# Kernel optimization log

Measured on AMD Instinct MI355X. Metric: run time of the kernel, lower is better.

The kernel has to match this reference:

```python
import jax, jax.numpy as jnp
import numpy as np

B, CS, CT, H, W = 16, 512, 512, 64, 64

def setup_inputs() -> dict:
    key = jax.random.key(0)
    k1, k2 = jax.random.split(key)
    x = jax.random.normal(k1, (B, CS, H, W), dtype=jnp.float32)
    # 16 Linear weights, each [out_ch, in_ch] (torch Linear layout), stacked
    Wg = jax.random.normal(k2, (16, CT, CS), dtype=jnp.float32) * (2.0 / CT) ** 0.5
    return {"x": x, "Wg": Wg}

def reference(x, Wg):
    # x: [B, Cs, H, W]; Wg: [16, Ct, Cs] indexed by phase r*4+c, r=(i%4), c=(j%4)
    # Dropout is identity in eval mode (deterministic reference).
    b, cs, h, w = x.shape
    ct = Wg.shape[1]
    Wrq = Wg.reshape(4, 4, ct, cs)               # [r, q, Ct, Cs]
    xr = x.reshape(b, cs, h // 4, 4, w // 4, 4)  # [b, c, h4, r, w4, q]
    # grouped matmul: each (r,q) phase uses its own weight
    out = jnp.einsum('bchrwq,rqoc->bohrwq', xr, Wrq)
    return out.reshape(b, ct, h, w)
```

## Files before the change

kernel.cpp:

```cpp
#include <hip/hip_runtime.h>
#include <stdint.h>


typedef __attribute__((ext_vector_type(8))) short short8;
typedef __attribute__((ext_vector_type(4))) float f32x4;

#define CS 512
#define CT 512
#define HW 4096
#define BK 32
#define MT 128
#define NR 8
#define ABYTES 32768
#define BBYTES 32768
#define BUFB (ABYTES + BBYTES)

__device__ __forceinline__ uint16_t f32_to_bf16(float f) {
    uint32_t u = __builtin_bit_cast(uint32_t, f);
    u += 0x7FFFu + ((u >> 16) & 1u);
    return (uint16_t)(u >> 16);
}

__global__ __launch_bounds__(256)
void w2_cvt(const float* __restrict__ Wg, uint16_t* __restrict__ W2) {
    int idx = (blockIdx.x * 256 + threadIdx.x) * 8;
    float4 a = *(const float4*)(Wg + idx);
    float4 b = *(const float4*)(Wg + idx + 4);
    uint16_t o[8];
    o[0]=f32_to_bf16(a.x); o[1]=f32_to_bf16(a.y); o[2]=f32_to_bf16(a.z); o[3]=f32_to_bf16(a.w);
    o[4]=f32_to_bf16(b.x); o[5]=f32_to_bf16(b.y); o[6]=f32_to_bf16(b.z); o[7]=f32_to_bf16(b.w);
    *(short8*)(W2 + idx) = *(short8*)o;
}

__global__ __launch_bounds__(256)
void xt_cvt(const float* __restrict__ x, uint16_t* __restrict__ xT) {
    const int c0 = blockIdx.x * 64;
    const int h  = blockIdx.y;
    const int b  = blockIdx.z;
    const int r = h & 3, h4 = h >> 2, rg = b * 16 + h4;
    __shared__ float L[64][65];
    const int tid = threadIdx.x;
    const int wr = tid & 15;
    const int cr = tid >> 4;
    const float* src = x + (((size_t)b * CS + c0 + cr) * 64 + h) * 64 + wr * 4;
    #pragma unroll
    for (int it = 0; it < 4; ++it) {
        float4 v = *(const float4*)(src + (size_t)it * 16 * HW);
        L[cr + it * 16][wr * 4 + 0] = v.x;
        L[cr + it * 16][wr * 4 + 1] = v.y;
        L[cr + it * 16][wr * 4 + 2] = v.z;
        L[cr + it * 16][wr * 4 + 3] = v.w;
    }
    __syncthreads();
    const int orow = tid >> 2;
    const int q = orow >> 4, w16 = orow & 15;
    const int cc = (tid & 3) * 16;
    const int w = w16 * 4 + q;
    uint16_t tmp[16];
    #pragma unroll
    for (int i = 0; i < 16; ++i) tmp[i] = f32_to_bf16(L[cc + i][w]);
    uint16_t* dst = xT + ((((size_t)(r * 4 + q) * 256 + rg) * 16 + w16) * 512 + c0 + cc);
    *(short8*)(dst)     = *(short8*)(tmp);
    *(short8*)(dst + 8) = *(short8*)(tmp + 8);
}

__global__ __launch_bounds__(512, 2)
void gwl_main(const uint16_t* __restrict__ W2, const uint16_t* __restrict__ xT,
              float* __restrict__ out) {
    const int nb = blockIdx.x;
    const int mb = blockIdx.y;
    const int r  = blockIdx.z;
    const int m0 = mb * MT;

    __shared__ __align__(16) unsigned char smem[2 * BUFB];
    float* T = (float*)smem;

    const int tid  = threadIdx.x;
    const int lane = tid & 63;
    const int wave = tid >> 6;
    const int q    = wave & 3;
    const int mw   = wave >> 2;
    const int lr = lane & 15, qd = lane >> 4;

    const int lrow = lane >> 2;
    const int swz  = ((lane & 3) ^ ((lane >> 3) & 3)) * 8;

    const uint16_t* abase = W2 + ((size_t)(r * 4 + q) * CT + m0 + mw * 64) * CS;
    const uint16_t* bbase = xT + (((size_t)(r * 4 + q) * 256 + nb * 8 + mw * 4) * 16) * 512;

    auto stage = [&](int k0, int bufn) {
        uint16_t* As = (uint16_t*)(smem + bufn * BUFB) + (q * 128 + mw * 64) * 32;
        uint16_t* Bs = (uint16_t*)(smem + bufn * BUFB + ABYTES) + (q * 128 + mw * 64) * 32;
        #pragma unroll
        for (int t = 0; t < 4; ++t) {
            const uint16_t* asrc = abase + (size_t)(t * 16 + lrow) * CS + k0 + swz;
            __builtin_amdgcn_global_load_lds(
                (const __attribute__((address_space(1))) void*)asrc,
                (__attribute__((address_space(3))) void*)(As + t * 512), 16, 0, 0);
        }
        #pragma unroll
        for (int t = 0; t < 4; ++t) {
            const uint16_t* bsrc = bbase + ((size_t)t * 16 + lrow) * 512 + k0 + swz;
            __builtin_amdgcn_global_load_lds(
                (const __attribute__((address_space(1))) void*)bsrc,
                (__attribute__((address_space(3))) void*)(Bs + t * 512), 16, 0, 0);
        }
    };

    f32x4 acc[4][8] = {};

    stage(0, 0);
    stage(BK, 1);
    asm volatile("s_waitcnt vmcnt(8)" ::: "memory");
    __builtin_amdgcn_s_barrier();

    const int rdswz = (qd ^ ((lr >> 1) & 3)) * 8;
    for (int k = 0; k < 16; ++k) {
        const int buf = k & 1;
        const uint16_t* Asq = (const uint16_t*)(smem + buf * BUFB)
                              + (q * 128 + mw * 64) * 32;
        const uint16_t* Bsq = (const uint16_t*)(smem + buf * BUFB + ABYTES)
                              + q * 128 * 32;
        short8 afr[4], bfr[8];
        #pragma unroll
        for (int i = 0; i < 4; ++i)
            afr[i] = *(const short8*)(Asq + (i * 16 + lr) * 32 + rdswz);
        #pragma unroll
        for (int j = 0; j < 8; ++j)
            bfr[j] = *(const short8*)(Bsq + (j * 16 + lr) * 32 + rdswz);
        asm volatile("s_waitcnt lgkmcnt(0)" ::: "memory");
        __builtin_amdgcn_sched_barrier(0);
        __builtin_amdgcn_s_barrier();
        if (k < 14) stage((k + 2) * BK, buf);

        __builtin_amdgcn_s_setprio(1);
        #pragma unroll
        for (int i = 0; i < 4; ++i)
            #pragma unroll
            for (int j = 0; j < 8; ++j)
                acc[i][j] = __builtin_amdgcn_mfma_f32_16x16x32_bf16(
                    afr[i], bfr[j], acc[i][j], 0, 0, 0);
        __builtin_amdgcn_s_setprio(0);

        if (k < 15) {
            if (k < 14) asm volatile("s_waitcnt vmcnt(8)" ::: "memory");
            else        asm volatile("s_waitcnt vmcnt(0)" ::: "memory");
            __builtin_amdgcn_s_barrier();
        }
    }

    const int m16s = tid >> 5;
    const int rs   = (tid >> 2) & 7;
    const int ws   = (tid & 3) * 16;
    const int rgs  = nb * NR + rs;
    const int obb  = rgs >> 4;
    const int oh4  = rgs & 15;
    #pragma unroll
    for (int ic = 0; ic < 8; ++ic) {
        __syncthreads();
        if (mw == (ic >> 2)) {
            const int i = ic & 3;
            #pragma unroll
            for (int j = 0; j < 8; ++j)
                #pragma unroll
                for (int g = 0; g < 4; ++g)
                    T[((qd * 4 + g) * 8 + j) * 68 + lr * 4 + q] = acc[i][j][g];
        }
        __syncthreads();
        float* op = out + ((size_t)obb * CT + m0 + ic * 16 + m16s) * HW
                        + (oh4 * 4 + r) * 64 + ws;
        const float* tp = T + (m16s * 8 + rs) * 68 + ws;
        #pragma unroll
        for (int c = 0; c < 4; ++c)
            ((float4*)op)[c] = ((const float4*)tp)[c];
    }
}

#define BPITCH 40
#define FBUFB 73728

__global__ __launch_bounds__(512, 2)
void gwl_fb(const float* __restrict__ x, const float* __restrict__ Wg,
            float* __restrict__ out) {
    const int nb = blockIdx.x, mb = blockIdx.y, r = blockIdx.z;
    const int m0 = mb * MT;
    __shared__ __align__(16) unsigned char smem[2 * FBUFB];
    float* T = (float*)smem;
    const int tid = threadIdx.x, lane = tid & 63, wave = tid >> 6;
    const int q = wave & 3, mw = wave >> 2;
    const int lr = lane & 15, qd = lane >> 4;
    const int w16 = tid & 15, rho = (tid >> 4) & 7, kw = tid >> 7;
    const int rg = nb * NR + rho, bb = rg >> 4, h4 = rg & 15;
    const float* bbase = x + (size_t)bb * CS * HW
                           + (size_t)((h4 * 4 + r) * 64 + w16 * 4);
    float4 breg[8];
    auto loadB = [&](int k0) {
        const float* p = bbase + (size_t)(k0 + kw * 8) * HW;
        #pragma unroll
        for (int cc = 0; cc < 8; ++cc) breg[cc] = *(const float4*)(p + (size_t)cc * HW);
    };
    auto writeB = [&](uint16_t* BsD) {
        #pragma unroll
        for (int qq = 0; qq < 4; ++qq) {
            uint16_t tmp[8];
            #pragma unroll
            for (int cc = 0; cc < 8; ++cc)
                tmp[cc] = f32_to_bf16(((const float*)&breg[cc])[qq]);
            *(short8*)(BsD + (qq * 128 + rho * 16 + w16) * BPITCH + kw * 8) = *(short8*)tmp;
        }
    };
    auto stageA = [&](int k0, uint16_t* AsD) {
        const int qa = tid >> 7, rem = tid & 127;
        const int ka = rem & 7, ma = rem >> 3;
        const float* ap = Wg + ((size_t)(r * 4 + qa) * CT + m0 + ma) * CS + k0 + ka * 4;
        const int kc = (((ka >> 1) ^ ((ma >> 1) & 3)) * 8) + (ka & 1) * 4;
        #pragma unroll
        for (int it = 0; it < 8; ++it) {
            float4 v = *(const float4*)(ap + (size_t)it * 16 * CS);
            uint16_t tmp[4] = {f32_to_bf16(v.x), f32_to_bf16(v.y),
                               f32_to_bf16(v.z), f32_to_bf16(v.w)};
            *(uint64_t*)(AsD + (qa * 128 + ma + it * 16) * 32 + kc) =
                *(const uint64_t*)tmp;
        }
    };
    f32x4 acc[4][8] = {};
    {
        uint16_t* As0 = (uint16_t*)smem;
        uint16_t* Bs0 = (uint16_t*)(smem + 32768);
        loadB(0);
        stageA(0, As0);
        writeB(Bs0);
        loadB(BK);
        __syncthreads();
    }
    for (int k = 0; k < 16; ++k) {
        const uint16_t* Asq = (const uint16_t*)(smem + (k & 1) * FBUFB)
                              + (q * 128 + mw * 64) * 32;
        const uint16_t* Bsq = (const uint16_t*)(smem + (k & 1) * FBUFB + 32768)
                              + q * 128 * BPITCH;
        short8 afr[4], bfr[8];
        #pragma unroll
        for (int i = 0; i < 4; ++i)
            afr[i] = *(const short8*)(Asq + (i * 16 + lr) * 32
                                      + ((qd ^ ((lr >> 1) & 3)) * 8));
        #pragma unroll
        for (int j = 0; j < 8; ++j)
            bfr[j] = *(const short8*)(Bsq + (j * 16 + lr) * BPITCH + qd * 8);
        if (k < 15) {
            uint16_t* AsN = (uint16_t*)(smem + ((k + 1) & 1) * FBUFB);
            uint16_t* BsN = (uint16_t*)(smem + ((k + 1) & 1) * FBUFB + 32768);
            stageA((k + 1) * BK, AsN);
            writeB(BsN);
            if (k < 14) loadB((k + 2) * BK);
        }
        #pragma unroll
        for (int i = 0; i < 4; ++i)
            #pragma unroll
            for (int j = 0; j < 8; ++j)
                acc[i][j] = __builtin_amdgcn_mfma_f32_16x16x32_bf16(
                    afr[i], bfr[j], acc[i][j], 0, 0, 0);
        if (k < 15) {
            asm volatile("s_waitcnt vmcnt(0)" ::: "memory");
            asm volatile("s_waitcnt lgkmcnt(0)" ::: "memory");
            __builtin_amdgcn_s_barrier();
        }
    }
    const int m16s = tid >> 5, rs = (tid >> 2) & 7, ws = (tid & 3) * 16;
    const int rgs = nb * NR + rs, obb = rgs >> 4, oh4 = rgs & 15;
    #pragma unroll
    for (int ic = 0; ic < 8; ++ic) {
        __syncthreads();
        if (mw == (ic >> 2)) {
            const int i = ic & 3;
            #pragma unroll
            for (int j = 0; j < 8; ++j)
                #pragma unroll
                for (int g = 0; g < 4; ++g)
                    T[((qd * 4 + g) * 8 + j) * 68 + lr * 4 + q] = acc[i][j][g];
        }
        __syncthreads();
        float* op = out + ((size_t)obb * CT + m0 + ic * 16 + m16s) * HW
                        + (oh4 * 4 + r) * 64 + ws;
        const float* tp = T + (m16s * 8 + rs) * 68 + ws;
        #pragma unroll
        for (int c = 0; c < 4; ++c)
            ((float4*)op)[c] = ((const float4*)tp)[c];
    }
}

extern "C" void kernel_launch(void* const* d_in, const int* in_sizes, int n_in,
                              void* d_out, int out_size, void* d_ws, size_t ws_size,
                              hipStream_t stream) {
    const float* x  = (const float*)d_in[0];
    const float* Wg = (const float*)d_in[1];
    float* out = (float*)d_out;
    dim3 grid(32, 4, 4);
    const size_t w2_elems = (size_t)16 * 512 * 512;
    const size_t xt_elems = (size_t)4 * 4 * 256 * 16 * 512;
    if (ws_size >= (w2_elems + xt_elems) * 2) {
        uint16_t* W2 = (uint16_t*)d_ws;
        uint16_t* xT = (uint16_t*)d_ws + w2_elems;
        w2_cvt<<<2048, 256, 0, stream>>>(Wg, W2);
        xt_cvt<<<dim3(8, 64, 16), 256, 0, stream>>>(x, xT);
        gwl_main<<<grid, 512, 0, stream>>>(W2, xT, out);
    } else {
        gwl_fb<<<grid, 512, 0, stream>>>(x, Wg, out);
    }
}
```

Before: 323.2 us.

## Load MFMA operands directly from global into registers, drop LDS staging

The main GEMM kernel no longer stages A/B tiles through double-buffered LDS with global_load_lds and barriers. Each wave now loads its bf16 fragments straight from global memory into registers with a two-deep register pipeline. The block shrinks to 256 threads with a 64-row M tile, and a linearized 1024-block grid is remapped to group blocks for L2 locality. This removes LDS traffic and barrier synchronisation but relies on caches for data reuse across waves and raises register pressure.

```diff
diff --git a/kernel.cpp b/kernel.cpp
--- a/kernel.cpp
+++ b/kernel.cpp
@@ -8,12 +8,6 @@
 #define CS 512
 #define CT 512
 #define HW 4096
-#define BK 32
-#define MT 128
-#define NR 8
-#define ABYTES 32768
-#define BBYTES 32768
-#define BUFB (ABYTES + BBYTES)
 
 __device__ __forceinline__ uint16_t f32_to_bf16(float f) {
     uint32_t u = __builtin_bit_cast(uint32_t, f);
@@ -64,118 +58,94 @@
     *(short8*)(dst + 8) = *(short8*)(tmp + 8);
 }
 
-__global__ __launch_bounds__(512, 2)
+__global__ __launch_bounds__(256, 2)
 void gwl_main(const uint16_t* __restrict__ W2, const uint16_t* __restrict__ xT,
               float* __restrict__ out) {
-    const int nb = blockIdx.x;
-    const int mb = blockIdx.y;
-    const int r  = blockIdx.z;
-    const int m0 = mb * MT;
-
-    __shared__ __align__(16) unsigned char smem[2 * BUFB];
-    float* T = (float*)smem;
+    const int l  = blockIdx.x;
+    const int x3 = l & 7;
+    const int t  = l >> 3;
+    const int mb = t >> 4;
+    const int combo = (t & 15) * 8 + x3;
+    const int nb = combo >> 2;
+    const int r  = combo & 3;
+    const int m0 = mb * 64;
 
     const int tid  = threadIdx.x;
     const int lane = tid & 63;
-    const int wave = tid >> 6;
-    const int q    = wave & 3;
-    const int mw   = wave >> 2;
+    const int q    = tid >> 6;
     const int lr = lane & 15, qd = lane >> 4;
 
-    const int lrow = lane >> 2;
-    const int swz  = ((lane & 3) ^ ((lane >> 3) & 3)) * 8;
-
-    const uint16_t* abase = W2 + ((size_t)(r * 4 + q) * CT + m0 + mw * 64) * CS;
-    const uint16_t* bbase = xT + (((size_t)(r * 4 + q) * 256 + nb * 8 + mw * 4) * 16) * 512;
-
-    auto stage = [&](int k0, int bufn) {
-        uint16_t* As = (uint16_t*)(smem + bufn * BUFB) + (q * 128 + mw * 64) * 32;
-        uint16_t* Bs = (uint16_t*)(smem + bufn * BUFB + ABYTES) + (q * 128 + mw * 64) * 32;
-        #pragma unroll
-        for (int t = 0; t < 4; ++t) {
-            const uint16_t* asrc = abase + (size_t)(t * 16 + lrow) * CS + k0 + swz;
-            __builtin_amdgcn_global_load_lds(
-                (const __attribute__((address_space(1))) void*)asrc,
-                (__attribute__((address_space(3))) void*)(As + t * 512), 16, 0, 0);
-        }
-        #pragma unroll
-        for (int t = 0; t < 4; ++t) {
-            const uint16_t* bsrc = bbase + ((size_t)t * 16 + lrow) * 512 + k0 + swz;
-            __builtin_amdgcn_global_load_lds(
-                (const __attribute__((address_space(1))) void*)bsrc,
-                (__attribute__((address_space(3))) void*)(Bs + t * 512), 16, 0, 0);
-        }
-    };
+    const uint16_t* Abase = W2 + ((size_t)(r * 4 + q) * CT + m0) * CS;
+    const uint16_t* Bbase = xT + ((size_t)(r * 4 + q) * 256 + nb * 8) * 16 * 512;
+    int voA[4], voB[8];
+    #pragma unroll
+    for (int i = 0; i < 4; ++i) voA[i] = (((i * 16 + lr) * CS) + qd * 8) * 2;
+    #pragma unroll
+    for (int j = 0; j < 8; ++j) voB[j] = (((j * 16 + lr) * 512) + qd * 8) * 2;
 
     f32x4 acc[4][8] = {};
-
-    stage(0, 0);
-    stage(BK, 1);
-    asm volatile("s_waitcnt vmcnt(8)" ::: "memory");
-    __builtin_amdgcn_s_barrier();
-
-    const int rdswz = (qd ^ ((lr >> 1) & 3)) * 8;
-    for (int k = 0; k < 16; ++k) {
-        const int buf = k & 1;
-        const uint16_t* Asq = (const uint16_t*)(smem + buf * BUFB)
-                              + (q * 128 + mw * 64) * 32;
-        const uint16_t* Bsq = (const uint16_t*)(smem + buf * BUFB + ABYTES)
-                              + q * 128 * 32;
-        short8 afr[4], bfr[8];
-        #pragma unroll
-        for (int i = 0; i < 4; ++i)
-            afr[i] = *(const short8*)(Asq + (i * 16 + lr) * 32 + rdswz);
+    short8 a0[4], b0[8], a1[4], b1[8];
+
+    auto LD = [&](short8* A, short8* B, int k) {
+        const int kb = k * 64;
+        #pragma unroll
+        for (int i = 0; i < 4; ++i)
+            A[i] = *(const short8*)((const char*)Abase + voA[i] + kb);
         #pragma unroll
         for (int j = 0; j < 8; ++j)
-            bfr[j] = *(const short8*)(Bsq + (j * 16 + lr) * 32 + rdswz);
-        asm volatile("s_waitcnt lgkmcnt(0)" ::: "memory");
-        __builtin_amdgcn_sched_barrier(0);
-        __builtin_amdgcn_s_barrier();
-        if (k < 14) stage((k + 2) * BK, buf);
-
-        __builtin_amdgcn_s_setprio(1);
+            B[j] = *(const short8*)((const char*)Bbase + voB[j] + kb);
+    };
+    auto FM = [&](const short8* A, const short8* B) {
         #pragma unroll
         for (int i = 0; i < 4; ++i)
             #pragma unroll
             for (int j = 0; j < 8; ++j)
                 acc[i][j] = __builtin_amdgcn_mfma_f32_16x16x32_bf16(
-                    afr[i], bfr[j], acc[i][j], 0, 0, 0);
-        __builtin_amdgcn_s_setprio(0);
-
-        if (k < 15) {
-            if (k < 14) asm volatile("s_waitcnt vmcnt(8)" ::: "memory");
-            else        asm volatile("s_waitcnt vmcnt(0)" ::: "memory");
-            __builtin_amdgcn_s_barrier();
-        }
-    }
-
-    const int m16s = tid >> 5;
-    const int rs   = (tid >> 2) & 7;
-    const int ws   = (tid & 3) * 16;
-    const int rgs  = nb * NR + rs;
+                    A[i], B[j], acc[i][j], 0, 0, 0);
+    };
+
+    LD(a0, b0, 0);
+    LD(a1, b1, 1);
+    #pragma unroll
+    for (int kp = 0; kp < 8; ++kp) {
+        if (kp < 7) {
+            FM(a0, b0); LD(a0, b0, 2 * kp + 2);
+            FM(a1, b1); LD(a1, b1, 2 * kp + 3);
+        } else {
+            FM(a0, b0);
+            FM(a1, b1);
+        }
+    }
+
+    __shared__ __align__(16) float T[16 * 8 * 68];
+    const int m16s = tid >> 4;
+    const int rsub = tid & 15;
+    const int rs   = rsub >> 1;
+    const int ws   = (rsub & 1) * 32;
+    const int rgs  = nb * 8 + rs;
     const int obb  = rgs >> 4;
     const int oh4  = rgs & 15;
     #pragma unroll
-    for (int ic = 0; ic < 8; ++ic) {
-        __syncthreads();
-        if (mw == (ic >> 2)) {
-            const int i = ic & 3;
-            #pragma unroll
-            for (int j = 0; j < 8; ++j)
-                #pragma unroll
-                for (int g = 0; g < 4; ++g)
-                    T[((qd * 4 + g) * 8 + j) * 68 + lr * 4 + q] = acc[i][j][g];
-        }
+    for (int ic = 0; ic < 4; ++ic) {
+        __syncthreads();
+        #pragma unroll
+        for (int j = 0; j < 8; ++j)
+            #pragma unroll
+            for (int g = 0; g < 4; ++g)
+                T[((qd * 4 + g) * 8 + j) * 68 + lr * 4 + q] = acc[ic][j][g];
         __syncthreads();
         float* op = out + ((size_t)obb * CT + m0 + ic * 16 + m16s) * HW
                         + (oh4 * 4 + r) * 64 + ws;
         const float* tp = T + (m16s * 8 + rs) * 68 + ws;
         #pragma unroll
-        for (int c = 0; c < 4; ++c)
+        for (int c = 0; c < 8; ++c)
             ((float4*)op)[c] = ((const float4*)tp)[c];
     }
 }
 
+#define MT 128
+#define NR 8
+#define BK 32
 #define BPITCH 40
 #define FBUFB 73728
 
@@ -294,7 +264,6 @@
     const float* x  = (const float*)d_in[0];
     const float* Wg = (const float*)d_in[1];
     float* out = (float*)d_out;
-    dim3 grid(32, 4, 4);
     const size_t w2_elems = (size_t)16 * 512 * 512;
     const size_t xt_elems = (size_t)4 * 4 * 256 * 16 * 512;
     if (ws_size >= (w2_elems + xt_elems) * 2) {
@@ -302,8 +271,8 @@
         uint16_t* xT = (uint16_t*)d_ws + w2_elems;
         w2_cvt<<<2048, 256, 0, stream>>>(Wg, W2);
         xt_cvt<<<dim3(8, 64, 16), 256, 0, stream>>>(x, xT);
-        gwl_main<<<grid, 512, 0, stream>>>(W2, xT, out);
+        gwl_main<<<1024, 256, 0, stream>>>(W2, xT, out);
     } else {
-        gwl_fb<<<grid, 512, 0, stream>>>(x, Wg, out);
-    }
-}
+        gwl_fb<<<dim3(32, 4, 4), 512, 0, stream>>>(x, Wg, out);
+    }
+}
```

New measurement: 373.8 us. 1.16x slower.
